# Kernel optimization log

Hardware: AMD Instinct MI355X
Metric: run time of the kernel (lower is better)

The kernel has to match this reference:

```python
import jax, jax.numpy as jnp
import numpy as np

N_NODES = 100000
N_EDGES = 1600000
F_IN = 128
EMB = 128
HEADS = 4
D_HEAD = EMB // HEADS
HIDDEN = 256
BATCH = 2048
CANDS = 16  # distractors + 1


def setup_inputs() -> dict:
    key = jax.random.key(0)
    ks = jax.random.split(key, 10)
    message = jax.random.normal(ks[0], (BATCH, HIDDEN), jnp.float32)
    x = jax.random.normal(ks[1], (N_NODES, F_IN), jnp.float32)
    edge_index = jax.random.randint(ks[2], (2, N_EDGES), 0, N_NODES, jnp.int64)
    indices = jax.random.randint(ks[3], (BATCH * CANDS,), 0, N_NODES, jnp.int64)
    s = 1.0 / np.sqrt(F_IN)
    W = jax.random.normal(ks[4], (F_IN, HEADS, D_HEAD), jnp.float32) * s
    att_src = jax.random.normal(ks[5], (HEADS, D_HEAD), jnp.float32) * s
    att_dst = jax.random.normal(ks[6], (HEADS, D_HEAD), jnp.float32) * s
    bias = jnp.zeros((EMB,), jnp.float32)
    fc_w = jax.random.normal(ks[7], (EMB, HIDDEN), jnp.float32) / np.sqrt(HIDDEN)
    fc_b = jnp.zeros((EMB,), jnp.float32)
    return {"message": message, "x": x, "edge_index": edge_index, "indices": indices,
            "W": W, "att_src": att_src, "att_dst": att_dst, "bias": bias,
            "fc_w": fc_w, "fc_b": fc_b}


def _gat(x, edge_index, W, att_src, att_dst, bias):
    N = x.shape[0]
    loops = jnp.arange(N, dtype=edge_index.dtype)
    src = jnp.concatenate([edge_index[0], loops])  # self-loops (PyG default)
    dst = jnp.concatenate([edge_index[1], loops])
    Wx = jnp.einsum('nf,fhd->nhd', x, W)                      # [N,H,D]
    a_s = (Wx * att_src).sum(-1)                              # [N,H]
    a_d = (Wx * att_dst).sum(-1)
    e = jax.nn.leaky_relu(a_s[src] + a_d[dst], 0.2)           # [E,H]
    m = jax.ops.segment_max(e, dst, num_segments=N)           # segment softmax
    ex = jnp.exp(e - m[dst])
    den = jax.ops.segment_sum(ex, dst, num_segments=N)
    alpha = ex / den[dst]
    out = jax.ops.segment_sum(alpha[:, :, None] * Wx[src], dst, num_segments=N)
    return out.reshape(N, -1) + bias                          # [N, H*D]


def reference(message, x, edge_index, indices, W, att_src, att_dst, bias, fc_w, fc_b):
    h = _gat(x, edge_index, W, att_src, att_dst, bias)        # [N, EMB]
    B = message.shape[0]
    emb = h[indices].reshape(B, -1, h.shape[-1])              # [B,C,EMB]
    msg = message @ fc_w.T + fc_b                             # [B,EMB]
    dots = jnp.einsum('bce,be->bc', emb, msg)                 # bmm scoring
    amax = jnp.abs(dots).max()
    tie = ((jnp.abs(dots) - amax) < 1e-10).astype(dots.dtype)
    noise = jax.random.normal(jax.random.key(42), dots.shape, dots.dtype)
    dots = dots + tie * amax * 1e-5 * noise
    return jax.nn.log_softmax(dots, axis=1)
```

## Files before the change

### kernel.cpp

```cpp
#include <hip/hip_runtime.h>
#include <stdint.h>
#include <stddef.h>

#define N_NODES 100000
#define N_EDGES 1600000
#define F_IN 128
#define EMB 128
#define HEADS 4
#define D_HEAD 32
#define HIDDEN 256
#define BATCH 2048
#define CANDS 16
#define NSLOTS 32768
#define WXBLOCKS 391
#define WTROWS 144
#define STR 136

typedef __attribute__((ext_vector_type(8))) short v8s;
typedef __attribute__((ext_vector_type(4))) float v4f;

__device__ __forceinline__ unsigned short f2bs(float f) {
  unsigned int u = __builtin_bit_cast(unsigned int, f);
  u = (u + 0x7fffu + ((u >> 16) & 1u)) >> 16;
  return (unsigned short)u;
}
__device__ __forceinline__ float bs2f(unsigned int s) {
  unsigned int u = (s & 0xffffu) << 16;
  return __builtin_bit_cast(float, u);
}

__global__ __launch_bounds__(256) void k_prep(const float* __restrict__ W,
                                              const float* __restrict__ att_src,
                                              const float* __restrict__ att_dst,
                                              unsigned short* __restrict__ Wtp,
                                              const int* __restrict__ idx,
                                              int* __restrict__ nidx,
                                              int* __restrict__ cnt) {
  int i = blockIdx.x * 256 + threadIdx.x;
  if (i < 128 * STR) {
    int r = i / STR, c = i - r * STR;
    Wtp[i] = (c < 128) ? f2bs(W[c * 128 + r]) : (unsigned short)0;
  } else if (i < WTROWS * STR) {
    int ii = i - 128 * STR;
    int r = ii / STR, c = ii - r * STR;
    unsigned short v = 0;
    if (c < 128 && r < 8) {
      const float* att = (r < 4) ? att_src : att_dst;
      int hh = r & 3;
      float s = 0.f;
#pragma unroll
      for (int d = 0; d < 32; ++d) s += W[c * 128 + hh * 32 + d] * att[hh * 32 + d];
      v = f2bs(s);
    }
    Wtp[i] = v;
  }
  if (i < NSLOTS) {
    cnt[i] = 0;
    nidx[idx[i]] = i;
  }
}

__global__ __launch_bounds__(256) void k_scatmsg(const int* __restrict__ ei,
                                                 const int* __restrict__ idx,
                                                 const int* __restrict__ nidx,
                                                 int* __restrict__ cnt,
                                                 int* __restrict__ srclist,
                                                 const float* __restrict__ message,
                                                 const float* __restrict__ fc_w,
                                                 const float* __restrict__ fc_b,
                                                 float* __restrict__ msg) {
  __shared__ float Sm[8][256];
  __shared__ float red[8 * 128];
  int tid = threadIdx.x;
  if (blockIdx.x < 256) {
    int b0 = blockIdx.x * 8;
    for (int i = tid; i < 8 * 256; i += 256)
      Sm[i >> 8][i & 255] = message[(size_t)b0 * 256 + i];
    __syncthreads();
    int e = tid & 127, half = tid >> 7;
    float acc[8];
#pragma unroll
    for (int r = 0; r < 8; ++r) acc[r] = 0.f;
    const float* wrow = fc_w + (size_t)e * 256 + half * 128;
    for (int k = 0; k < 128; k += 4) {
      float4 w4 = *(const float4*)(wrow + k);
#pragma unroll
      for (int r = 0; r < 8; ++r) {
        float4 m4 = *(const float4*)(&Sm[r][half * 128 + k]);
        acc[r] += m4.x * w4.x + m4.y * w4.y + m4.z * w4.z + m4.w * w4.w;
      }
    }
    __syncthreads();
    if (half == 0) {
#pragma unroll
      for (int r = 0; r < 8; ++r) red[r * 128 + e] = acc[r];
    }
    __syncthreads();
    if (half == 1) {
#pragma unroll
      for (int r = 0; r < 8; ++r) red[r * 128 + e] += acc[r];
    }
    __syncthreads();
    for (int i = tid; i < 1024; i += 256)
      msg[(size_t)b0 * 128 + i] = red[i] + fc_b[i & 127];
  } else {
    int e = (blockIdx.x - 256) * 256 + tid;
    if (e >= N_EDGES) return;
    int dst = ei[N_EDGES + e];
    unsigned int ni = (unsigned int)nidx[dst];
    if (ni >= NSLOTS) return;
    if (idx[ni] != dst) return;
    int pos = atomicAdd(&cnt[ni], 1);
    if (pos < 64) srclist[ni * 64 + pos] = ei[e];
  }
}

__global__ __launch_bounds__(256) void k_wx(const float* __restrict__ x,
                                            const unsigned short* __restrict__ Wtp,
                                            unsigned short* __restrict__ Wx,
                                            float* __restrict__ a_s,
                                            float* __restrict__ a_d) {
  __shared__ unsigned short wt[WTROWS * STR];
  __shared__ unsigned short xs[64 * STR];
  int tid = threadIdx.x;

  {
    const uint4* s = (const uint4*)Wtp;
    uint4* d = (uint4*)wt;
#pragma unroll
    for (int it = 0; it < 10; ++it) {
      int i = it * 256 + tid;
      if (i < WTROWS * STR / 8) d[i] = s[i];
    }
  }

  int w = tid >> 6, lane = tid & 63;
  int m = lane & 15, quad = lane >> 4;

  for (int chunk = 0; chunk < 4; ++chunk) {
    int rbase = blockIdx.x * 256 + chunk * 64;

    float4 f[8];
#pragma unroll
    for (int it = 0; it < 4; ++it) {
      int cid = it * 256 + tid;
      int row = cid >> 4, c = cid & 15;
      int gr = rbase + row;
      if (gr >= N_NODES) gr = N_NODES - 1;
      const float4* gp = (const float4*)(x + (size_t)gr * 128 + c * 8);
      f[2 * it] = gp[0];
      f[2 * it + 1] = gp[1];
    }
#pragma unroll
    for (int it = 0; it < 4; ++it) {
      int cid = it * 256 + tid;
      int row = cid >> 4, c = cid & 15;
      float4 f0 = f[2 * it], f1 = f[2 * it + 1];
      v8s a;
      a[0] = (short)f2bs(f0.x); a[1] = (short)f2bs(f0.y);
      a[2] = (short)f2bs(f0.z); a[3] = (short)f2bs(f0.w);
      a[4] = (short)f2bs(f1.x); a[5] = (short)f2bs(f1.y);
      a[6] = (short)f2bs(f1.z); a[7] = (short)f2bs(f1.w);
      *(v8s*)(&xs[row * STR + c * 8]) = a;
    }
    __syncthreads();

    v8s afrag[4];
#pragma unroll
    for (int t = 0; t < 4; ++t)
      afrag[t] = *(const v8s*)(&xs[(w * 16 + m) * STR + t * 32 + quad * 8]);

    v4f acc[9];
#pragma unroll
    for (int nt = 0; nt < 9; ++nt) {
      v4f a0 = {0.f, 0.f, 0.f, 0.f};
      const unsigned short* brow = wt + (size_t)(nt * 16 + m) * STR;
#pragma unroll
      for (int t = 0; t < 4; ++t) {
        v8s b = *(const v8s*)(brow + t * 32 + quad * 8);
        a0 = __builtin_amdgcn_mfma_f32_16x16x32_bf16(afrag[t], b, a0, 0, 0, 0);
      }
      acc[nt] = a0;
    }

#pragma unroll
    for (int r = 0; r < 4; ++r) {
      int orow = rbase + w * 16 + quad * 4 + r;
      if (orow < N_NODES) {
        if (m < 4) a_s[(size_t)orow * 4 + m] = acc[8][r];
        else if (m < 8) a_d[(size_t)orow * 4 + m - 4] = acc[8][r];
      }
    }

    __syncthreads();
#pragma unroll
    for (int nt = 0; nt < 8; ++nt)
#pragma unroll
      for (int r = 0; r < 4; ++r)
        xs[(w * 16 + quad * 4 + r) * STR + nt * 16 + m] = f2bs(acc[nt][r]);
    asm volatile("s_waitcnt lgkmcnt(0)" ::: "memory");
#pragma unroll
    for (int j = 0; j < 4; ++j) {
      int fr = 4 * j + (lane >> 4);
      int fc = (lane & 15) * 8;
      int grow = rbase + w * 16 + fr;
      v8s v = *(const v8s*)(&xs[(w * 16 + fr) * STR + fc]);
      if (grow < N_NODES) *(v8s*)(&Wx[(size_t)grow * 128 + fc]) = v;
    }
    __syncthreads();
  }
}

__global__ __launch_bounds__(256) void k_agg(const float* __restrict__ a_s,
                                             const float* __restrict__ a_d,
                                             const unsigned short* __restrict__ Wx,
                                             const int* __restrict__ idx,
                                             const int* __restrict__ nidx,
                                             const int* __restrict__ cnt,
                                             const int* __restrict__ srclist,
                                             const int* __restrict__ ei,
                                             const float* __restrict__ bias,
                                             unsigned short* __restrict__ hout) {
  __shared__ int sS[16][64];
  __shared__ float sW[16][64 * 4];
  int w = threadIdx.x >> 6, lane = threadIdx.x & 63;
  int q = lane >> 4, li = lane & 15;
  int wq = w * 4 + q;
  int wid = (blockIdx.x * 4 + w) * 4 + q;
  int dst = idx[wid];
  bool act = (nidx[dst] == wid);
  int degRaw = 0, deg = 0;
  float4 ad4 = {0.f, 0.f, 0.f, 0.f};
  float4 dsum = {0.f, 0.f, 0.f, 0.f};
  if (act) {
    degRaw = cnt[wid];
    deg = degRaw < 64 ? degRaw : 64;
    ad4 = *(const float4*)(a_d + (size_t)dst * 4);
    for (int t = li; t < deg; t += 16) {
      int sv = srclist[wid * 64 + t];
      float4 as = *(const float4*)(a_s + (size_t)sv * 4);
      float e0 = as.x + ad4.x; e0 = e0 > 0.f ? e0 : 0.2f * e0;
      float e1 = as.y + ad4.y; e1 = e1 > 0.f ? e1 : 0.2f * e1;
      float e2 = as.z + ad4.z; e2 = e2 > 0.f ? e2 : 0.2f * e2;
      float e3 = as.w + ad4.w; e3 = e3 > 0.f ? e3 : 0.2f * e3;
      float4 w4;
      w4.x = __expf(e0); w4.y = __expf(e1);
      w4.z = __expf(e2); w4.w = __expf(e3);
      sS[wq][t] = sv;
      *(float4*)(&sW[wq][t * 4]) = w4;
      dsum.x += w4.x; dsum.y += w4.y; dsum.z += w4.z; dsum.w += w4.w;
    }
  }
  __syncthreads();
  if (!act) return;

#pragma unroll
  for (int o = 8; o >= 1; o >>= 1) {
    dsum.x += __shfl_xor(dsum.x, o);
    dsum.y += __shfl_xor(dsum.y, o);
    dsum.z += __shfl_xor(dsum.z, o);
    dsum.w += __shfl_xor(dsum.w, o);
  }

  int hh = li >> 2;
  float4 as4 = *(const float4*)(a_s + (size_t)dst * 4);
  float s0 = as4.x + ad4.x; s0 = s0 > 0.f ? s0 : 0.2f * s0;
  float s1 = as4.y + ad4.y; s1 = s1 > 0.f ? s1 : 0.2f * s1;
  float s2 = as4.z + ad4.z; s2 = s2 > 0.f ? s2 : 0.2f * s2;
  float s3 = as4.w + ad4.w; s3 = s3 > 0.f ? s3 : 0.2f * s3;
  float w0 = __expf(s0), w1 = __expf(s1), w2 = __expf(s2), w3 = __expf(s3);
  float wSelf = hh < 2 ? (hh == 0 ? w0 : w1) : (hh == 2 ? w2 : w3);
  float denE = hh < 2 ? (hh == 0 ? dsum.x : dsum.y) : (hh == 2 ? dsum.z : dsum.w);
  float den = denE + wSelf;

  float acc[8];
  {
    uint4 u = *(const uint4*)(Wx + (size_t)dst * 128 + li * 8);
    acc[0] = wSelf * bs2f(u.x); acc[1] = wSelf * bs2f(u.x >> 16);
    acc[2] = wSelf * bs2f(u.y); acc[3] = wSelf * bs2f(u.y >> 16);
    acc[4] = wSelf * bs2f(u.z); acc[5] = wSelf * bs2f(u.z >> 16);
    acc[6] = wSelf * bs2f(u.w); acc[7] = wSelf * bs2f(u.w >> 16);
  }

  if (degRaw > 64) {
    float adH = hh < 2 ? (hh == 0 ? ad4.x : ad4.y) : (hh == 2 ? ad4.z : ad4.w);
    den = wSelf;
    for (int e = 0; e < N_EDGES; ++e) {
      if (ei[N_EDGES + e] == dst) {
        int sv = ei[e];
        float ash = a_s[(size_t)sv * 4 + hh];
        float ee = ash + adH; ee = ee > 0.f ? ee : 0.2f * ee;
        float wA = __expf(ee);
        den += wA;
        uint4 u = *(const uint4*)(Wx + (size_t)sv * 128 + li * 8);
        acc[0] += wA * bs2f(u.x); acc[1] += wA * bs2f(u.x >> 16);
        acc[2] += wA * bs2f(u.y); acc[3] += wA * bs2f(u.y >> 16);
        acc[4] += wA * bs2f(u.z); acc[5] += wA * bs2f(u.z >> 16);
        acc[6] += wA * bs2f(u.w); acc[7] += wA * bs2f(u.w >> 16);
      }
    }
  } else {
#pragma unroll 4
    for (int j = 0; j < deg; ++j) {
      int s = sS[wq][j];
      float wA = sW[wq][j * 4 + hh];
      uint4 u = *(const uint4*)(Wx + (size_t)s * 128 + li * 8);
      acc[0] += wA * bs2f(u.x); acc[1] += wA * bs2f(u.x >> 16);
      acc[2] += wA * bs2f(u.y); acc[3] += wA * bs2f(u.y >> 16);
      acc[4] += wA * bs2f(u.z); acc[5] += wA * bs2f(u.z >> 16);
      acc[6] += wA * bs2f(u.w); acc[7] += wA * bs2f(u.w >> 16);
    }
  }

  float inv = 1.0f / den;
  float4 b0 = *(const float4*)(bias + li * 8);
  float4 b1 = *(const float4*)(bias + li * 8 + 4);
  uint4 o;
  o.x = (unsigned int)f2bs(acc[0] * inv + b0.x)
      | ((unsigned int)f2bs(acc[1] * inv + b0.y) << 16);
  o.y = (unsigned int)f2bs(acc[2] * inv + b0.z)
      | ((unsigned int)f2bs(acc[3] * inv + b0.w) << 16);
  o.z = (unsigned int)f2bs(acc[4] * inv + b1.x)
      | ((unsigned int)f2bs(acc[5] * inv + b1.y) << 16);
  o.w = (unsigned int)f2bs(acc[6] * inv + b1.z)
      | ((unsigned int)f2bs(acc[7] * inv + b1.w) << 16);
  *(uint4*)(hout + (size_t)dst * 128 + li * 8) = o;
}

__global__ __launch_bounds__(256) void k_score(const float* __restrict__ msg,
                                               const unsigned short* __restrict__ h,
                                               const int* __restrict__ indices,
                                               float* __restrict__ out) {
  __shared__ float Sm[8 * 128];
  __shared__ float sp[128];
  int tid = threadIdx.x;
  int b0 = blockIdx.x * 8;
  for (int i = tid; i < 1024; i += 256) Sm[i] = msg[(size_t)b0 * 128 + i];
  __syncthreads();

  int r = (tid & 127) >> 4, c = tid & 15, half = tid >> 7;
  int id = indices[(b0 + r) * 16 + c];
  const unsigned short* hr = h + (size_t)id * 128 + half * 64;
  const float* mr = Sm + r * 128 + half * 64;
  float dot = 0.f;
#pragma unroll
  for (int k = 0; k < 64; k += 8) {
    uint4 qv = *(const uint4*)(hr + k);
    float4 m0 = *(const float4*)(mr + k);
    float4 m1 = *(const float4*)(mr + k + 4);
    dot += bs2f(qv.x) * m0.x + bs2f(qv.x >> 16) * m0.y
         + bs2f(qv.y) * m0.z + bs2f(qv.y >> 16) * m0.w
         + bs2f(qv.z) * m1.x + bs2f(qv.z >> 16) * m1.y
         + bs2f(qv.w) * m1.z + bs2f(qv.w >> 16) * m1.w;
  }
  if (half == 1) sp[tid - 128] = dot;
  __syncthreads();
  if (half == 0) {
    dot += sp[tid];
    float mx = dot;
#pragma unroll
    for (int o = 1; o < 16; o <<= 1) mx = fmaxf(mx, __shfl_xor(mx, o));
    float ex = __expf(dot - mx);
    float sum = ex;
#pragma unroll
    for (int o = 1; o < 16; o <<= 1) sum += __shfl_xor(sum, o);
    float lse = mx + __logf(sum);
    out[(b0 + r) * 16 + c] = dot - lse;
  }
}

extern "C" void kernel_launch(void* const* d_in, const int* in_sizes, int n_in,
                              void* d_out, int out_size, void* d_ws, size_t ws_size,
                              hipStream_t stream) {
  (void)in_sizes; (void)n_in; (void)out_size; (void)ws_size;
  const float* message = (const float*)d_in[0];
  const float* x       = (const float*)d_in[1];
  const int*   ei      = (const int*)d_in[2];
  const int*   indices = (const int*)d_in[3];
  const float* W       = (const float*)d_in[4];
  const float* att_src = (const float*)d_in[5];
  const float* att_dst = (const float*)d_in[6];
  const float* bias    = (const float*)d_in[7];
  const float* fc_w    = (const float*)d_in[8];
  const float* fc_b    = (const float*)d_in[9];
  float* out = (float*)d_out;

  char* p = (char*)d_ws;
  auto alloc = [&](size_t bytes) -> char* {
    char* r = p;
    p += (bytes + 255) & ~(size_t)255;
    return r;
  };
  unsigned short* Wx = (unsigned short*)alloc((size_t)N_NODES * 128 * 2);
  unsigned short* h  = (unsigned short*)alloc((size_t)N_NODES * 128 * 2);
  float* a_s = (float*)alloc((size_t)N_NODES * 4 * 4);
  float* a_d = (float*)alloc((size_t)N_NODES * 4 * 4);
  unsigned short* Wtp = (unsigned short*)alloc((size_t)WTROWS * STR * 2);
  int* nidx      = (int*)alloc((size_t)N_NODES * 4);
  int* cnt       = (int*)alloc((size_t)NSLOTS * 4);
  int* srclist   = (int*)alloc((size_t)NSLOTS * 64 * 4);
  float* msg     = (float*)alloc((size_t)BATCH * 128 * 4);

  k_prep<<<128, 256, 0, stream>>>(W, att_src, att_dst, Wtp, indices, nidx, cnt);
  k_scatmsg<<<256 + N_EDGES / 256, 256, 0, stream>>>(ei, indices, nidx, cnt, srclist,
                                                     message, fc_w, fc_b, msg);
  k_wx<<<WXBLOCKS, 256, 0, stream>>>(x, Wtp, Wx, a_s, a_d);
  k_agg<<<NSLOTS / 16, 256, 0, stream>>>(a_s, a_d, Wx, indices, nidx, cnt, srclist, ei, bias, h);
  k_score<<<BATCH / 8, 256, 0, stream>>>(msg, h, indices, out);
}
```

Baseline: 179.1 us.

## Fuse GAT aggregation with candidate scoring and load x fragments directly

The aggregation kernel now computes each candidate's embedding and dots it with the message row in registers, then does the per-batch log-softmax in the same block. This removes the h buffer write and the separate scoring kernel. Duplicate candidate nodes are no longer deduplicated, so any node that appears more than once is aggregated again. Separately, k_wx loads x rows straight into MFMA A fragments instead of staging them through shared memory, which removes two barriers per chunk but gives up coalesced staging.

```diff
diff --git a/kernel.cpp b/kernel.cpp
--- a/kernel.cpp
+++ b/kernel.cpp
@@ -133,42 +133,29 @@
       if (i < WTROWS * STR / 8) d[i] = s[i];
     }
   }
+  __syncthreads();
 
   int w = tid >> 6, lane = tid & 63;
   int m = lane & 15, quad = lane >> 4;
 
   for (int chunk = 0; chunk < 4; ++chunk) {
     int rbase = blockIdx.x * 256 + chunk * 64;
-
-    float4 f[8];
-#pragma unroll
-    for (int it = 0; it < 4; ++it) {
-      int cid = it * 256 + tid;
-      int row = cid >> 4, c = cid & 15;
-      int gr = rbase + row;
-      if (gr >= N_NODES) gr = N_NODES - 1;
-      const float4* gp = (const float4*)(x + (size_t)gr * 128 + c * 8);
-      f[2 * it] = gp[0];
-      f[2 * it + 1] = gp[1];
-    }
-#pragma unroll
-    for (int it = 0; it < 4; ++it) {
-      int cid = it * 256 + tid;
-      int row = cid >> 4, c = cid & 15;
-      float4 f0 = f[2 * it], f1 = f[2 * it + 1];
+    int gr = rbase + w * 16 + m;
+    if (gr >= N_NODES) gr = N_NODES - 1;
+    const float* xrow = x + (size_t)gr * 128;
+
+    v8s afrag[4];
+#pragma unroll
+    for (int t = 0; t < 4; ++t) {
+      const float4* gp = (const float4*)(xrow + t * 32 + quad * 8);
+      float4 f0 = gp[0], f1 = gp[1];
       v8s a;
       a[0] = (short)f2bs(f0.x); a[1] = (short)f2bs(f0.y);
       a[2] = (short)f2bs(f0.z); a[3] = (short)f2bs(f0.w);
       a[4] = (short)f2bs(f1.x); a[5] = (short)f2bs(f1.y);
       a[6] = (short)f2bs(f1.z); a[7] = (short)f2bs(f1.w);
-      *(v8s*)(&xs[row * STR + c * 8]) = a;
-    }
-    __syncthreads();
-
-    v8s afrag[4];
-#pragma unroll
-    for (int t = 0; t < 4; ++t)
-      afrag[t] = *(const v8s*)(&xs[(w * 16 + m) * STR + t * 32 + quad * 8]);
+      afrag[t] = a;
+    }
 
     v4f acc[9];
 #pragma unroll
@@ -192,7 +179,6 @@
       }
     }
 
-    __syncthreads();
 #pragma unroll
     for (int nt = 0; nt < 8; ++nt)
 #pragma unroll
@@ -207,52 +193,49 @@
       v8s v = *(const v8s*)(&xs[(w * 16 + fr) * STR + fc]);
       if (grow < N_NODES) *(v8s*)(&Wx[(size_t)grow * 128 + fc]) = v;
     }
-    __syncthreads();
-  }
-}
-
-__global__ __launch_bounds__(256) void k_agg(const float* __restrict__ a_s,
-                                             const float* __restrict__ a_d,
-                                             const unsigned short* __restrict__ Wx,
-                                             const int* __restrict__ idx,
-                                             const int* __restrict__ nidx,
-                                             const int* __restrict__ cnt,
-                                             const int* __restrict__ srclist,
-                                             const int* __restrict__ ei,
-                                             const float* __restrict__ bias,
-                                             unsigned short* __restrict__ hout) {
+  }
+}
+
+__global__ __launch_bounds__(256) void k_aggscore(const float* __restrict__ a_s,
+                                                  const float* __restrict__ a_d,
+                                                  const unsigned short* __restrict__ Wx,
+                                                  const int* __restrict__ idx,
+                                                  const int* __restrict__ nidx,
+                                                  const int* __restrict__ cnt,
+                                                  const int* __restrict__ srclist,
+                                                  const int* __restrict__ ei,
+                                                  const float* __restrict__ bias,
+                                                  const float* __restrict__ msg,
+                                                  float* __restrict__ out) {
   __shared__ int sS[16][64];
   __shared__ float sW[16][64 * 4];
+  __shared__ float sdots[16];
   int w = threadIdx.x >> 6, lane = threadIdx.x & 63;
   int q = lane >> 4, li = lane & 15;
   int wq = w * 4 + q;
-  int wid = (blockIdx.x * 4 + w) * 4 + q;
+  int b = blockIdx.x;
+  int wid = b * 16 + wq;
   int dst = idx[wid];
-  bool act = (nidx[dst] == wid);
-  int degRaw = 0, deg = 0;
-  float4 ad4 = {0.f, 0.f, 0.f, 0.f};
+  int ci = nidx[dst];
+  int degRaw = cnt[ci];
+  int deg = degRaw < 64 ? degRaw : 64;
+  float4 ad4 = *(const float4*)(a_d + (size_t)dst * 4);
   float4 dsum = {0.f, 0.f, 0.f, 0.f};
-  if (act) {
-    degRaw = cnt[wid];
-    deg = degRaw < 64 ? degRaw : 64;
-    ad4 = *(const float4*)(a_d + (size_t)dst * 4);
-    for (int t = li; t < deg; t += 16) {
-      int sv = srclist[wid * 64 + t];
-      float4 as = *(const float4*)(a_s + (size_t)sv * 4);
-      float e0 = as.x + ad4.x; e0 = e0 > 0.f ? e0 : 0.2f * e0;
-      float e1 = as.y + ad4.y; e1 = e1 > 0.f ? e1 : 0.2f * e1;
-      float e2 = as.z + ad4.z; e2 = e2 > 0.f ? e2 : 0.2f * e2;
-      float e3 = as.w + ad4.w; e3 = e3 > 0.f ? e3 : 0.2f * e3;
-      float4 w4;
-      w4.x = __expf(e0); w4.y = __expf(e1);
-      w4.z = __expf(e2); w4.w = __expf(e3);
-      sS[wq][t] = sv;
-      *(float4*)(&sW[wq][t * 4]) = w4;
-      dsum.x += w4.x; dsum.y += w4.y; dsum.z += w4.z; dsum.w += w4.w;
-    }
-  }
-  __syncthreads();
-  if (!act) return;
+  for (int t = li; t < deg; t += 16) {
+    int sv = srclist[ci * 64 + t];
+    float4 as = *(const float4*)(a_s + (size_t)sv * 4);
+    float e0 = as.x + ad4.x; e0 = e0 > 0.f ? e0 : 0.2f * e0;
+    float e1 = as.y + ad4.y; e1 = e1 > 0.f ? e1 : 0.2f * e1;
+    float e2 = as.z + ad4.z; e2 = e2 > 0.f ? e2 : 0.2f * e2;
+    float e3 = as.w + ad4.w; e3 = e3 > 0.f ? e3 : 0.2f * e3;
+    float4 w4;
+    w4.x = __expf(e0); w4.y = __expf(e1);
+    w4.z = __expf(e2); w4.w = __expf(e3);
+    sS[wq][t] = sv;
+    *(float4*)(&sW[wq][t * 4]) = w4;
+    dsum.x += w4.x; dsum.y += w4.y; dsum.z += w4.z; dsum.w += w4.w;
+  }
+  asm volatile("s_waitcnt lgkmcnt(0)" ::: "memory");
 
 #pragma unroll
   for (int o = 8; o >= 1; o >>= 1) {
@@ -315,57 +298,27 @@
   float inv = 1.0f / den;
   float4 b0 = *(const float4*)(bias + li * 8);
   float4 b1 = *(const float4*)(bias + li * 8 + 4);
-  uint4 o;
-  o.x = (unsigned int)f2bs(acc[0] * inv + b0.x)
-      | ((unsigned int)f2bs(acc[1] * inv + b0.y) << 16);
-  o.y = (unsigned int)f2bs(acc[2] * inv + b0.z)
-      | ((unsigned int)f2bs(acc[3] * inv + b0.w) << 16);
-  o.z = (unsigned int)f2bs(acc[4] * inv + b1.x)
-      | ((unsigned int)f2bs(acc[5] * inv + b1.y) << 16);
-  o.w = (unsigned int)f2bs(acc[6] * inv + b1.z)
-      | ((unsigned int)f2bs(acc[7] * inv + b1.w) << 16);
-  *(uint4*)(hout + (size_t)dst * 128 + li * 8) = o;
-}
-
-__global__ __launch_bounds__(256) void k_score(const float* __restrict__ msg,
-                                               const unsigned short* __restrict__ h,
-                                               const int* __restrict__ indices,
-                                               float* __restrict__ out) {
-  __shared__ float Sm[8 * 128];
-  __shared__ float sp[128];
-  int tid = threadIdx.x;
-  int b0 = blockIdx.x * 8;
-  for (int i = tid; i < 1024; i += 256) Sm[i] = msg[(size_t)b0 * 128 + i];
+  const float* mrow = msg + (size_t)b * 128 + li * 8;
+  float4 m0 = *(const float4*)(mrow);
+  float4 m1 = *(const float4*)(mrow + 4);
+  float dp = (acc[0] * inv + b0.x) * m0.x + (acc[1] * inv + b0.y) * m0.y
+           + (acc[2] * inv + b0.z) * m0.z + (acc[3] * inv + b0.w) * m0.w
+           + (acc[4] * inv + b1.x) * m1.x + (acc[5] * inv + b1.y) * m1.y
+           + (acc[6] * inv + b1.z) * m1.z + (acc[7] * inv + b1.w) * m1.w;
+#pragma unroll
+  for (int o = 8; o >= 1; o >>= 1) dp += __shfl_xor(dp, o);
+  if (li == 0) sdots[wq] = dp;
   __syncthreads();
-
-  int r = (tid & 127) >> 4, c = tid & 15, half = tid >> 7;
-  int id = indices[(b0 + r) * 16 + c];
-  const unsigned short* hr = h + (size_t)id * 128 + half * 64;
-  const float* mr = Sm + r * 128 + half * 64;
-  float dot = 0.f;
-#pragma unroll
-  for (int k = 0; k < 64; k += 8) {
-    uint4 qv = *(const uint4*)(hr + k);
-    float4 m0 = *(const float4*)(mr + k);
-    float4 m1 = *(const float4*)(mr + k + 4);
-    dot += bs2f(qv.x) * m0.x + bs2f(qv.x >> 16) * m0.y
-         + bs2f(qv.y) * m0.z + bs2f(qv.y >> 16) * m0.w
-         + bs2f(qv.z) * m1.x + bs2f(qv.z >> 16) * m1.y
-         + bs2f(qv.w) * m1.z + bs2f(qv.w >> 16) * m1.w;
-  }
-  if (half == 1) sp[tid - 128] = dot;
-  __syncthreads();
-  if (half == 0) {
-    dot += sp[tid];
-    float mx = dot;
+  if (threadIdx.x < 16) {
+    float d = sdots[threadIdx.x];
+    float mx = d;
 #pragma unroll
     for (int o = 1; o < 16; o <<= 1) mx = fmaxf(mx, __shfl_xor(mx, o));
-    float ex = __expf(dot - mx);
+    float ex = __expf(d - mx);
     float sum = ex;
 #pragma unroll
     for (int o = 1; o < 16; o <<= 1) sum += __shfl_xor(sum, o);
-    float lse = mx + __logf(sum);
-    out[(b0 + r) * 16 + c] = dot - lse;
+    out[b * 16 + threadIdx.x] = d - mx - __logf(sum);
   }
 }
 
@@ -392,7 +345,6 @@
     return r;
   };
   unsigned short* Wx = (unsigned short*)alloc((size_t)N_NODES * 128 * 2);
-  unsigned short* h  = (unsigned short*)alloc((size_t)N_NODES * 128 * 2);
   float* a_s = (float*)alloc((size_t)N_NODES * 4 * 4);
   float* a_d = (float*)alloc((size_t)N_NODES * 4 * 4);
   unsigned short* Wtp = (unsigned short*)alloc((size_t)WTROWS * STR * 2);
@@ -405,6 +357,6 @@
   k_scatmsg<<<256 + N_EDGES / 256, 256, 0, stream>>>(ei, indices, nidx, cnt, srclist,
                                                      message, fc_w, fc_b, msg);
   k_wx<<<WXBLOCKS, 256, 0, stream>>>(x, Wtp, Wx, a_s, a_d);
-  k_agg<<<NSLOTS / 16, 256, 0, stream>>>(a_s, a_d, Wx, indices, nidx, cnt, srclist, ei, bias, h);
-  k_score<<<BATCH / 8, 256, 0, stream>>>(msg, h, indices, out);
-}
+  k_aggscore<<<BATCH, 256, 0, stream>>>(a_s, a_d, Wx, indices, nidx, cnt, srclist,
+                                        ei, bias, msg, out);
+}
```

Result: no change. 180.9 us (+1.0%).
